# Kernel optimization log

Hardware: AMD Instinct MI355X
Metric: run time of the kernel (lower is better)

The kernel has to match this reference:

```python
import jax, jax.numpy as jnp
import numpy as np

E = 1024   # emb_dim
H = 1024   # hidden_size
L = 2      # num_layers
V = 50257  # vocab_size
S = 2048   # encoder input length
T = 2048   # decoder target length


def setup_inputs() -> dict:
    key = jax.random.key(0)
    ks = jax.random.split(key, 16)
    s = 0.02  # init scale
    f32 = jnp.float32
    return {
        "inputs": jax.random.randint(ks[0], (1, S), 0, V),
        "outputs": jax.random.randint(ks[1], (1, T), 0, V),
        "sos": 1,
        "enc_emb": jax.random.normal(ks[2], (V, E), f32) * s,
        "dec_emb": jax.random.normal(ks[3], (V, E), f32) * s,
        # Stacked LSTM weights; layer-0 input dim == E == H so layers stack.
        "enc_Wih": jax.random.normal(ks[4], (L, 4 * H, H), f32) * s,
        "enc_Whh": jax.random.normal(ks[5], (L, 4 * H, H), f32) * s,
        "enc_bih": jax.random.normal(ks[6], (L, 4 * H), f32) * s,
        "enc_bhh": jax.random.normal(ks[7], (L, 4 * H), f32) * s,
        "dec_Wih": jax.random.normal(ks[8], (L, 4 * H, H), f32) * s,
        "dec_Whh": jax.random.normal(ks[9], (L, 4 * H, H), f32) * s,
        "dec_bih": jax.random.normal(ks[10], (L, 4 * H), f32) * s,
        "dec_bhh": jax.random.normal(ks[11], (L, 4 * H), f32) * s,
        "lin_W": jax.random.normal(ks[12], (V, H), f32) * s,
        "lin_b": jax.random.normal(ks[13], (V,), f32) * s,
    }


def _run_stack(xs, Wih, Whh, bih, bhh, h0, c0):
    # xs: [S, E]; Wih/Whh: [L, 4H, H]; h0/c0: [L, H]
    # PyTorch LSTM gate order: i, f, g, o.
    h_fin, c_fin = [], []
    for l in range(Wih.shape[0]):
        Wi, Wh, bi, bh = Wih[l], Whh[l], bih[l], bhh[l]

        def step(carry, x, Wi=Wi, Wh=Wh, bi=bi, bh=bh):
            h, c = carry
            g = Wi @ x + bi + Wh @ h + bh           # [4H]
            i, f, gg, o = jnp.split(g, 4)
            c = jax.nn.sigmoid(f) * c + jax.nn.sigmoid(i) * jnp.tanh(gg)
            h = jax.nn.sigmoid(o) * jnp.tanh(c)
            return (h, c), h

        (h, c), xs = jax.lax.scan(step, (h0[l], c0[l]), xs)
        h_fin.append(h)
        c_fin.append(c)
    return xs, jnp.stack(h_fin), jnp.stack(c_fin)


def reference(inputs, outputs, sos, enc_emb, dec_emb,
              enc_Wih, enc_Whh, enc_bih, enc_bhh,
              dec_Wih, dec_Whh, dec_bih, dec_bhh,
              lin_W, lin_b):
    # Encoder over the source sequence (batch == 1, squeezed away).
    x = enc_emb[inputs[0]]                       # [S, E]
    z = jnp.zeros((L, H), dtype=x.dtype)
    _, hN, cN = _run_stack(x, enc_Wih, enc_Whh, enc_bih, enc_bhh, z, z)
    # Full teacher forcing: decoder inputs are [sos, outputs[:, :-1]].
    dec_tokens = jnp.concatenate(
        [jnp.array([sos], dtype=outputs.dtype), outputs[0, :-1]])
    y = dec_emb[dec_tokens]                      # [T, E]
    dec_out, _, _ = _run_stack(y, dec_Wih, dec_Whh, dec_bih, dec_bhh, hN, cN)
    logits = dec_out @ lin_W.T + lin_b           # [T, V]
    return logits
```

## Files before the change

kernel.cpp:

```cpp
#include <hip/hip_runtime.h>
#include <hip/hip_bf16.h>
#include <math.h>

#define S_LEN 2048
#define T_LEN 2048
#define HID   1024
#define GATES 4096
#define VOCAB 50257
#define SPINCAP 262144

typedef unsigned int u32;
typedef unsigned long long ull;
typedef u32 u32x4 __attribute__((ext_vector_type(4)));
typedef float f32x4 __attribute__((ext_vector_type(4)));

__device__ __forceinline__ float fsig_(float x)  { return 1.0f / (1.0f + __expf(-x)); }
__device__ __forceinline__ float ftanh_(float x) { float e = __expf(2.0f * x); return 1.0f - 2.0f / (e + 1.0f); }

__device__ __forceinline__ u32x4 cload16(const ull* p) {
  u32x4 v;
  asm volatile("global_load_dwordx4 %0, %1, off sc0 sc1\n\ts_waitcnt vmcnt(0)"
               : "=v"(v) : "v"(p) : "memory");
  return v;
}

__device__ __forceinline__ u32x4 pollslots(const ull* p, u32 want) {
  u32x4 v = cload16(p);
  int n = 0;
  while (v.y < want || v.w < want) {
    if (++n > SPINCAP) break;
    v = cload16(p);
  }
  return v;
}

__global__ void zero_f4(float4* __restrict__ p, size_t n4) {
  size_t i = (size_t)blockIdx.x * blockDim.x + threadIdx.x;
  size_t stride = (size_t)gridDim.x * blockDim.x;
  for (; i < n4; i += stride) p[i] = make_float4(0.f, 0.f, 0.f, 0.f);
}

__global__ void build_dec_tokens(const int* __restrict__ outputs, const int* __restrict__ sos,
                                 int* __restrict__ toks, int T) {
  int t = blockIdx.x * blockDim.x + threadIdx.x;
  if (t < T) toks[t] = (t == 0) ? sos[0] : outputs[t - 1];
}

__global__ __launch_bounds__(256) void gemm_xwt(
    const float* __restrict__ X, const float* __restrict__ W,
    const float* __restrict__ b1,
    float* __restrict__ C, int M, int N, int K)
{
  __shared__ float Xs[16][68];
  __shared__ float Ws[16][68];
  const int tid = threadIdx.x;
  const int tx = tid & 15;
  const int ty = tid >> 4;
  const int m0 = blockIdx.y * 64;
  const int n0 = blockIdx.x * 64;
  const int lr = tid >> 2;
  const int lc = (tid & 3) * 4;
  float acc[4][4] = {{0.f}};

  for (int k0 = 0; k0 < K; k0 += 16) {
    float4 xv = *(const float4*)(X + (size_t)(m0 + lr) * K + k0 + lc);
    float4 wv = make_float4(0.f, 0.f, 0.f, 0.f);
    int wr = n0 + lr;
    if (wr < N) wv = *(const float4*)(W + (size_t)wr * K + k0 + lc);
    __syncthreads();
    Xs[lc + 0][lr] = xv.x; Xs[lc + 1][lr] = xv.y; Xs[lc + 2][lr] = xv.z; Xs[lc + 3][lr] = xv.w;
    Ws[lc + 0][lr] = wv.x; Ws[lc + 1][lr] = wv.y; Ws[lc + 2][lr] = wv.z; Ws[lc + 3][lr] = wv.w;
    __syncthreads();
#pragma unroll
    for (int kk = 0; kk < 16; ++kk) {
      float4 a = *(const float4*)&Xs[kk][ty * 4];
      float4 b = *(const float4*)&Ws[kk][tx * 4];
      float av[4] = {a.x, a.y, a.z, a.w};
      float bv[4] = {b.x, b.y, b.z, b.w};
#pragma unroll
      for (int i = 0; i < 4; ++i)
#pragma unroll
        for (int j = 0; j < 4; ++j)
          acc[i][j] = fmaf(av[i], bv[j], acc[i][j]);
    }
  }
#pragma unroll
  for (int i = 0; i < 4; ++i) {
    int m = m0 + ty * 4 + i;
#pragma unroll
    for (int j = 0; j < 4; ++j) {
      int n = n0 + tx * 4 + j;
      if (n < N) C[(size_t)m * N + n] = acc[i][j] + (b1 ? b1[n] : 0.f);
    }
  }
}

__global__ __launch_bounds__(512, 1) void lstm2(
    const float* __restrict__ emb,  const int* __restrict__ toks,
    const float* __restrict__ Wi0,  const float* __restrict__ Wh0,
    const float* __restrict__ bi0,  const float* __restrict__ bh0,
    const float* __restrict__ Wi1,  const float* __restrict__ Wh1,
    const float* __restrict__ bi1,  const float* __restrict__ bh1,
    const float* __restrict__ h00,  const float* __restrict__ c00,
    const float* __restrict__ h01,  const float* __restrict__ c01,
    ull* __restrict__ s0, ull* __restrict__ s1,
    float* __restrict__ hf0, float* __restrict__ cf0,
    float* __restrict__ hf1, float* __restrict__ cf1,
    float* __restrict__ dec_out, int T)
{
  const int tid = threadIdx.x;
  const int wg  = blockIdx.x;
  const bool isL0 = (wg < 128);
  const int wgl = isL0 ? wg : wg - 128;

  const int lane16 = tid & 15;
  const int rloc = tid >> 4;
  const int jloc = rloc & 7;
  const int gate = rloc >> 3;
  const int grow = gate * HID + wgl * 8 + jloc;

  __shared__ float lds_x[2][HID];
  __shared__ float lds_h[HID];
  __shared__ float lds_g[32];
  __shared__ float lds_c[8];

  const float* Wi = isL0 ? Wi0 : Wi1;
  const float* Wh = isL0 ? Wh0 : Wh1;
  const float breg = (isL0 ? (bi0[grow] + bh0[grow]) : (bi1[grow] + bh1[grow]));

  f32x4 Wir[16], Whr[16];
  {
    const f32x4* wi = (const f32x4*)(Wi + (size_t)grow * HID);
    const f32x4* wh = (const f32x4*)(Wh + (size_t)grow * HID);
#pragma unroll
    for (int i = 0; i < 16; ++i) {
      Wir[i] = wi[lane16 + i * 16];
      Whr[i] = wh[lane16 + i * 16];
    }
  }
#pragma unroll
  for (int i = 0; i < 16; ++i)
    asm volatile("" : "+v"(Wir[i]), "+v"(Whr[i]));

  {
    const float* hini = isL0 ? h00 : h01;
    const float* cini = isL0 ? c00 : c01;
    if (tid < 8) lds_c[tid] = cini[wgl * 8 + tid];
    if (tid < 256) ((float4*)lds_h)[tid] = ((const float4*)hini)[tid];
    if (isL0 && tid < 256) {
      int tok = toks[0];
      ((float4*)lds_x[0])[tid] = ((const float4*)(emb + (size_t)tok * HID))[tid];
    }
  }
  __syncthreads();

  ull* s_mine = isL0 ? s0 : s1;

  for (int t = 0; t < T; ++t) {
    const int cur = t & 1;

    if (isL0) {
      if (t > 0) {
        const ull* ph = s0 + (size_t)(t - 1) * HID + 2 * tid;
        u32x4 v = pollslots(ph, (u32)t);
        lds_h[2 * tid]     = __uint_as_float(v.x);
        lds_h[2 * tid + 1] = __uint_as_float(v.z);
      }
    } else {
      {
        const ull* px = s0 + (size_t)t * HID + 2 * tid;
        u32x4 v = pollslots(px, (u32)(t + 1));
        lds_x[0][2 * tid]     = __uint_as_float(v.x);
        lds_x[0][2 * tid + 1] = __uint_as_float(v.z);
      }
      if (t > 0) {
        const ull* ph = s1 + (size_t)(t - 1) * HID + 2 * tid;
        u32x4 v = pollslots(ph, (u32)t);
        lds_h[2 * tid]     = __uint_as_float(v.x);
        lds_h[2 * tid + 1] = __uint_as_float(v.z);
      }
    }
    __syncthreads();

    if (isL0 && tid < 256 && t + 1 < T) {
      int tok = toks[t + 1];
      ((float4*)lds_x[cur ^ 1])[tid] = ((const float4*)(emb + (size_t)tok * HID))[tid];
    }

    const float* xbuf = isL0 ? lds_x[cur] : lds_x[0];
    float p0 = 0.f, p1 = 0.f, p2 = 0.f, p3 = 0.f;
#pragma unroll
    for (int i = 0; i < 16; ++i) {
      const float4 xv = *(const float4*)&xbuf[(lane16 << 2) + (i << 6)];
      p0 = fmaf(Wir[i].x, xv.x, p0);
      p1 = fmaf(Wir[i].y, xv.y, p1);
      p2 = fmaf(Wir[i].z, xv.z, p2);
      p3 = fmaf(Wir[i].w, xv.w, p3);
    }
#pragma unroll
    for (int i = 0; i < 16; ++i) {
      const float4 hv = *(const float4*)&lds_h[(lane16 << 2) + (i << 6)];
      p0 = fmaf(Whr[i].x, hv.x, p0);
      p1 = fmaf(Whr[i].y, hv.y, p1);
      p2 = fmaf(Whr[i].z, hv.z, p2);
      p3 = fmaf(Whr[i].w, hv.w, p3);
    }
    float sum = (p0 + p1) + (p2 + p3);
    sum += __shfl_xor(sum, 1);
    sum += __shfl_xor(sum, 2);
    sum += __shfl_xor(sum, 4);
    sum += __shfl_xor(sum, 8);
    if (lane16 == 0) lds_g[rloc] = sum + breg;
    __syncthreads();

    if (tid < 8) {
      const float gi = lds_g[tid];
      const float gf = lds_g[8 + tid];
      const float gg = lds_g[16 + tid];
      const float go = lds_g[24 + tid];
      const float c = fsig_(gf) * lds_c[tid] + fsig_(gi) * ftanh_(gg);
      const float h = fsig_(go) * ftanh_(c);
      lds_c[tid] = c;
      const int col = wgl * 8 + tid;
      const ull pk = ((ull)(u32)(t + 1) << 32) | (ull)__float_as_uint(h);
      __hip_atomic_store(&s_mine[(size_t)t * HID + col], pk,
                         __ATOMIC_RELAXED, __HIP_MEMORY_SCOPE_AGENT);
      if (!isL0 && dec_out) dec_out[(size_t)t * HID + col] = h;
      if (t == T - 1) {
        if (isL0) { if (hf0) hf0[col] = h; if (cf0) cf0[col] = c; }
        else      { if (hf1) hf1[col] = h; if (cf1) cf1[col] = c; }
      }
    }
  }
}

extern "C" void kernel_launch(void* const* d_in, const int* in_sizes, int n_in,
                              void* d_out, int out_size, void* d_ws, size_t ws_size,
                              hipStream_t stream) {
  const int*   inputs  = (const int*)d_in[0];
  const int*   outputs = (const int*)d_in[1];
  const int*   sos     = (const int*)d_in[2];
  const float* enc_emb = (const float*)d_in[3];
  const float* dec_emb = (const float*)d_in[4];
  const float* enc_Wih = (const float*)d_in[5];
  const float* enc_Whh = (const float*)d_in[6];
  const float* enc_bih = (const float*)d_in[7];
  const float* enc_bhh = (const float*)d_in[8];
  const float* dec_Wih = (const float*)d_in[9];
  const float* dec_Whh = (const float*)d_in[10];
  const float* dec_bih = (const float*)d_in[11];
  const float* dec_bhh = (const float*)d_in[12];
  const float* lin_W   = (const float*)d_in[13];
  const float* lin_b   = (const float*)d_in[14];

  float* out = (float*)d_out;
  ull* s0e = (ull*)d_out;
  ull* s1e = s0e + 2097152;
  ull* s0d = s1e + 2097152;
  ull* s1d = s0d + 2097152;

  char* ws = (char*)d_ws;
  float* zerosv = (float*)(ws + 0);
  float* hf0    = (float*)(ws + 4096);
  float* cf0    = (float*)(ws + 8192);
  float* hf1    = (float*)(ws + 12288);
  float* cf1    = (float*)(ws + 16384);
  int*   dtoks  = (int*)(ws + 20480);
  float* B2     = (float*)(ws + ((size_t)1 << 20));

  const size_t WOFF = (size_t)GATES * HID;

  zero_f4<<<2048, 256, 0, stream>>>((float4*)d_out, 4194304);
  zero_f4<<<1, 256, 0, stream>>>((float4*)zerosv, 256);
  build_dec_tokens<<<8, 256, 0, stream>>>(outputs, sos, dtoks, T_LEN);

  lstm2<<<256, 512, 0, stream>>>(
      enc_emb, inputs,
      enc_Wih, enc_Whh, enc_bih, enc_bhh,
      enc_Wih + WOFF, enc_Whh + WOFF, enc_bih + GATES, enc_bhh + GATES,
      zerosv, zerosv, zerosv, zerosv,
      s0e, s1e, hf0, cf0, hf1, cf1, nullptr, S_LEN);

  lstm2<<<256, 512, 0, stream>>>(
      dec_emb, dtoks,
      dec_Wih, dec_Whh, dec_bih, dec_bhh,
      dec_Wih + WOFF, dec_Whh + WOFF, dec_bih + GATES, dec_bhh + GATES,
      hf0, cf0, hf1, cf1,
      s0d, s1d, nullptr, nullptr, nullptr, nullptr, B2, T_LEN);

  dim3 gemmV_grid((VOCAB + 63) / 64, T_LEN / 64);
  gemm_xwt<<<gemmV_grid, 256, 0, stream>>>(B2, lin_W, lin_b, out, T_LEN, VOCAB, HID);
}
```

Before: 15.93 ms.

## Remap LSTM step so each wave owns one hidden unit with weights in AGPRs

```diff
diff --git a/kernel.cpp b/kernel.cpp
--- a/kernel.cpp
+++ b/kernel.cpp
@@ -32,6 +32,17 @@
     v = cload16(p);
   }
   return v;
+}
+
+__device__ __forceinline__ void poll2(const ull* pa, const ull* pb, u32 wa, u32 wb,
+                                      u32x4& va, u32x4& vb) {
+  asm volatile("global_load_dwordx4 %0, %2, off sc0 sc1\n\t"
+               "global_load_dwordx4 %1, %3, off sc0 sc1\n\t"
+               "s_waitcnt vmcnt(0)"
+               : "=&v"(va), "=&v"(vb) : "v"(pa), "v"(pb) : "memory");
+  int n = 0;
+  while (va.y < wa || va.w < wa) { if (++n > SPINCAP) break; va = cload16(pa); }
+  while (vb.y < wb || vb.w < wb) { if (++n > SPINCAP) break; vb = cload16(pb); }
 }
 
 __global__ void zero_f4(float4* __restrict__ p, size_t n4) {
@@ -108,44 +119,43 @@
     float* __restrict__ hf1, float* __restrict__ cf1,
     float* __restrict__ dec_out, int T)
 {
-  const int tid = threadIdx.x;
-  const int wg  = blockIdx.x;
+  const int tid   = threadIdx.x;
+  const int wg    = blockIdx.x;
   const bool isL0 = (wg < 128);
-  const int wgl = isL0 ? wg : wg - 128;
-
-  const int lane16 = tid & 15;
-  const int rloc = tid >> 4;
-  const int jloc = rloc & 7;
-  const int gate = rloc >> 3;
-  const int grow = gate * HID + wgl * 8 + jloc;
+  const int wgl   = isL0 ? wg : wg - 128;
+  const int wlane = tid & 63;
+  const int unit  = tid >> 6;
 
   __shared__ float lds_x[2][HID];
   __shared__ float lds_h[HID];
-  __shared__ float lds_g[32];
-  __shared__ float lds_c[8];
 
   const float* Wi = isL0 ? Wi0 : Wi1;
   const float* Wh = isL0 ? Wh0 : Wh1;
-  const float breg = (isL0 ? (bi0[grow] + bh0[grow]) : (bi1[grow] + bh1[grow]));
-
-  f32x4 Wir[16], Whr[16];
-  {
-    const f32x4* wi = (const f32x4*)(Wi + (size_t)grow * HID);
-    const f32x4* wh = (const f32x4*)(Wh + (size_t)grow * HID);
-#pragma unroll
-    for (int i = 0; i < 16; ++i) {
-      Wir[i] = wi[lane16 + i * 16];
-      Whr[i] = wh[lane16 + i * 16];
-    }
-  }
-#pragma unroll
-  for (int i = 0; i < 16; ++i)
-    asm volatile("" : "+v"(Wir[i]), "+v"(Whr[i]));
-
+  const float* bi = isL0 ? bi0 : bi1;
+  const float* bh = isL0 ? bh0 : bh1;
+
+  float bias[4];
+  float Awt[128];
+#pragma unroll
+  for (int r = 0; r < 4; ++r) {
+    const int growr = r * HID + wgl * 8 + unit;
+    bias[r] = bi[growr] + bh[growr];
+    const float* wiR = Wi + (size_t)growr * HID;
+    const float* whR = Wh + (size_t)growr * HID;
+#pragma unroll
+    for (int k = 0; k < 8; ++k) {
+      const float* src = (k < 4) ? wiR : whR;
+      f32x4 w = *(const f32x4*)(src + 4 * (64 * (k & 3) + wlane));
+      asm volatile("v_accvgpr_write_b32 %0, %1" : "=a"(Awt[r * 32 + k * 4 + 0]) : "v"(w.x));
+      asm volatile("v_accvgpr_write_b32 %0, %1" : "=a"(Awt[r * 32 + k * 4 + 1]) : "v"(w.y));
+      asm volatile("v_accvgpr_write_b32 %0, %1" : "=a"(Awt[r * 32 + k * 4 + 2]) : "v"(w.z));
+      asm volatile("v_accvgpr_write_b32 %0, %1" : "=a"(Awt[r * 32 + k * 4 + 3]) : "v"(w.w));
+    }
+  }
+
+  float creg = (isL0 ? c00 : c01)[wgl * 8 + unit];
   {
     const float* hini = isL0 ? h00 : h01;
-    const float* cini = isL0 ? c00 : c01;
-    if (tid < 8) lds_c[tid] = cini[wgl * 8 + tid];
     if (tid < 256) ((float4*)lds_h)[tid] = ((const float4*)hini)[tid];
     if (isL0 && tid < 256) {
       int tok = toks[0];
@@ -161,23 +171,24 @@
 
     if (isL0) {
       if (t > 0) {
-        const ull* ph = s0 + (size_t)(t - 1) * HID + 2 * tid;
-        u32x4 v = pollslots(ph, (u32)t);
+        u32x4 v = pollslots(s0 + (size_t)(t - 1) * HID + 2 * tid, (u32)t);
         lds_h[2 * tid]     = __uint_as_float(v.x);
         lds_h[2 * tid + 1] = __uint_as_float(v.z);
       }
     } else {
-      {
-        const ull* px = s0 + (size_t)t * HID + 2 * tid;
-        u32x4 v = pollslots(px, (u32)(t + 1));
+      if (t == 0) {
+        u32x4 v = pollslots(s0 + 2 * tid, 1u);
         lds_x[0][2 * tid]     = __uint_as_float(v.x);
         lds_x[0][2 * tid + 1] = __uint_as_float(v.z);
-      }
-      if (t > 0) {
-        const ull* ph = s1 + (size_t)(t - 1) * HID + 2 * tid;
-        u32x4 v = pollslots(ph, (u32)t);
-        lds_h[2 * tid]     = __uint_as_float(v.x);
-        lds_h[2 * tid + 1] = __uint_as_float(v.z);
+      } else {
+        u32x4 vx, vh;
+        poll2(s0 + (size_t)t * HID + 2 * tid,
+              s1 + (size_t)(t - 1) * HID + 2 * tid,
+              (u32)(t + 1), (u32)t, vx, vh);
+        lds_x[0][2 * tid]     = __uint_as_float(vx.x);
+        lds_x[0][2 * tid + 1] = __uint_as_float(vx.z);
+        lds_h[2 * tid]       = __uint_as_float(vh.x);
+        lds_h[2 * tid + 1]   = __uint_as_float(vh.z);
       }
     }
     __syncthreads();
@@ -188,49 +199,57 @@
     }
 
     const float* xbuf = isL0 ? lds_x[cur] : lds_x[0];
-    float p0 = 0.f, p1 = 0.f, p2 = 0.f, p3 = 0.f;
-#pragma unroll
-    for (int i = 0; i < 16; ++i) {
-      const float4 xv = *(const float4*)&xbuf[(lane16 << 2) + (i << 6)];
-      p0 = fmaf(Wir[i].x, xv.x, p0);
-      p1 = fmaf(Wir[i].y, xv.y, p1);
-      p2 = fmaf(Wir[i].z, xv.z, p2);
-      p3 = fmaf(Wir[i].w, xv.w, p3);
-    }
-#pragma unroll
-    for (int i = 0; i < 16; ++i) {
-      const float4 hv = *(const float4*)&lds_h[(lane16 << 2) + (i << 6)];
-      p0 = fmaf(Whr[i].x, hv.x, p0);
-      p1 = fmaf(Whr[i].y, hv.y, p1);
-      p2 = fmaf(Whr[i].z, hv.z, p2);
-      p3 = fmaf(Whr[i].w, hv.w, p3);
-    }
-    float sum = (p0 + p1) + (p2 + p3);
-    sum += __shfl_xor(sum, 1);
-    sum += __shfl_xor(sum, 2);
-    sum += __shfl_xor(sum, 4);
-    sum += __shfl_xor(sum, 8);
-    if (lane16 == 0) lds_g[rloc] = sum + breg;
-    __syncthreads();
-
-    if (tid < 8) {
-      const float gi = lds_g[tid];
-      const float gf = lds_g[8 + tid];
-      const float gg = lds_g[16 + tid];
-      const float go = lds_g[24 + tid];
-      const float c = fsig_(gf) * lds_c[tid] + fsig_(gi) * ftanh_(gg);
-      const float h = fsig_(go) * ftanh_(c);
-      lds_c[tid] = c;
-      const int col = wgl * 8 + tid;
+    float4 xh[8];
+#pragma unroll
+    for (int k = 0; k < 4; ++k) xh[k]     = ((const float4*)xbuf)[64 * k + wlane];
+#pragma unroll
+    for (int k = 0; k < 4; ++k) xh[4 + k] = ((const float4*)lds_h)[64 * k + wlane];
+
+    float sr[4];
+#pragma unroll
+    for (int r = 0; r < 4; ++r) {
+      float acc = 0.f;
+#pragma unroll
+      for (int k = 0; k < 8; ++k) {
+        float w0, w1, w2, w3;
+        asm volatile("v_accvgpr_read_b32 %0, %1" : "=v"(w0) : "a"(Awt[r * 32 + k * 4 + 0]));
+        asm volatile("v_accvgpr_read_b32 %0, %1" : "=v"(w1) : "a"(Awt[r * 32 + k * 4 + 1]));
+        asm volatile("v_accvgpr_read_b32 %0, %1" : "=v"(w2) : "a"(Awt[r * 32 + k * 4 + 2]));
+        asm volatile("v_accvgpr_read_b32 %0, %1" : "=v"(w3) : "a"(Awt[r * 32 + k * 4 + 3]));
+        acc = fmaf(w0, xh[k].x, acc);
+        acc = fmaf(w1, xh[k].y, acc);
+        acc = fmaf(w2, xh[k].z, acc);
+        acc = fmaf(w3, xh[k].w, acc);
+      }
+      sr[r] = acc;
+    }
+
+#pragma unroll
+    for (int r = 0; r < 4; ++r) {
+      float v = sr[r];
+      v += __shfl_xor(v, 1);
+      v += __shfl_xor(v, 2);
+      v += __shfl_xor(v, 4);
+      v += __shfl_xor(v, 8);
+      v += __shfl_xor(v, 16);
+      v += __shfl_xor(v, 32);
+      sr[r] = v + bias[r];
+    }
+
+    creg = fsig_(sr[1]) * creg + fsig_(sr[0]) * ftanh_(sr[2]);
+    const float h = fsig_(sr[3]) * ftanh_(creg);
+    if (wlane == 0) {
+      const int col = wgl * 8 + unit;
       const ull pk = ((ull)(u32)(t + 1) << 32) | (ull)__float_as_uint(h);
       __hip_atomic_store(&s_mine[(size_t)t * HID + col], pk,
                          __ATOMIC_RELAXED, __HIP_MEMORY_SCOPE_AGENT);
       if (!isL0 && dec_out) dec_out[(size_t)t * HID + col] = h;
       if (t == T - 1) {
-        if (isL0) { if (hf0) hf0[col] = h; if (cf0) cf0[col] = c; }
-        else      { if (hf1) hf1[col] = h; if (cf1) cf1[col] = c; }
+        if (isL0) { if (hf0) hf0[col] = h; if (cf0) cf0[col] = creg; }
+        else      { if (hf1) hf1[col] = h; if (cf1) cf1[col] = creg; }
       }
     }
+    __syncthreads();
   }
 }
 
```

New measurement: 16.20 ms. No clear change (+1.7%).
